# Optimization experiments

Measured on AMD Instinct MI355X. Metric: run time of the kernel, lower is better.

The kernel has to match this reference:

```python
import jax, jax.numpy as jnp
import numpy as np

EPS = 1e-6
NUM_HEADS = 8
NUM_TOKENS = 196

def setup_inputs() -> dict:
    key = jax.random.key(0)
    ks = jax.random.split(key, 4)
    B, N, C = 32, 3136, 384
    H, Dh, M = NUM_HEADS, C // NUM_HEADS, NUM_TOKENS
    return {
        "x": jax.random.normal(ks[0], (B, N, C), dtype=jnp.float32),
        "q_param": jax.random.normal(ks[1], (1, M, H, Dh), dtype=jnp.float32) * 0.02,
        "kv_w": jax.random.normal(ks[2], (2 * C, C), dtype=jnp.float32) * 0.02,
        "proj_w": jax.random.normal(ks[3], (C, C), dtype=jnp.float32) * 0.02,
        "proj_b": jnp.zeros((C,), dtype=jnp.float32),
        "ln_w": jnp.ones((C,), dtype=jnp.float32),
        "ln_b": jnp.zeros((C,), dtype=jnp.float32),
    }

def reference(x, q_param, kv_w, proj_w, proj_b, ln_w, ln_b):
    B, N, C = x.shape
    H = NUM_HEADS
    Dh = C // H
    # LayerNorm (eps=1e-6)
    mu = jnp.mean(x, axis=-1, keepdims=True)
    var = jnp.mean(jnp.square(x - mu), axis=-1, keepdims=True)
    x = (x - mu) * jax.lax.rsqrt(var + EPS) * ln_w + ln_b
    # exact GELU (nn.GELU default)
    x = jax.nn.gelu(x, approximate=False)
    # kv projection (no bias): [B,N,2C] -> k,v each [B,H,N,Dh]
    kv = (x @ kv_w.T).reshape(B, N, 2, H, Dh)
    kv = jnp.transpose(kv, (2, 0, 3, 1, 4))
    k, v = kv[0], kv[1]
    # learnable queries: (1,M,H,Dh) -> (1,H,M,Dh)
    q = jnp.transpose(q_param, (0, 2, 1, 3))
    # NOTE: source applies NO 1/sqrt(Dh) scaling
    attn = jnp.einsum("bhmd,bhnd->bhmn", jnp.broadcast_to(q, (B, H, NUM_TOKENS, Dh)), k)
    attn = jax.nn.softmax(attn, axis=-1)
    out = jnp.einsum("bhmn,bhnd->bhmd", attn, v)  # [B,H,M,Dh]
    out = jnp.transpose(out, (0, 2, 1, 3)).reshape(B, NUM_TOKENS, C)
    return out @ proj_w.T + proj_b
```

## Files before the change

### kernel.cpp

```cpp
#include <hip/hip_runtime.h>
#include <stdint.h>

typedef float f32x4 __attribute__((ext_vector_type(4)));
typedef short s16x8 __attribute__((ext_vector_type(8)));
typedef short s16x4 __attribute__((ext_vector_type(4)));
typedef unsigned short ushort_t;

#define B_  32
#define N_  3136
#define C_  384
#define H_  8
#define DH_ 48
#define M_  196
#define ROWS  (B_*N_)
#define PROWS (B_*M_)

static __device__ __forceinline__ ushort_t f2bf(float f) {
  union { float f; uint32_t u; } v; v.f = f;
  uint32_t r = (v.u + 0x7fffu + ((v.u >> 16) & 1u)) >> 16;
  return (ushort_t)r;
}
static __device__ __forceinline__ ushort_t f2bf_fast(float f) {
  union { float f; uint32_t u; } v; v.f = f;
  return (ushort_t)((v.u + 0x8000u) >> 16);
}

static __device__ __forceinline__ f32x4 mfma_16x16x32(s16x8 a, s16x8 b, f32x4 c) {
  return __builtin_amdgcn_mfma_f32_16x16x32_bf16(a, b, c, 0, 0, 0);
}

static __device__ __forceinline__ f32x4 mfma_16x16x16(s16x4 a, s16x4 b, f32x4 c) {
#if __has_builtin(__builtin_amdgcn_mfma_f32_16x16x16_bf16)
  return __builtin_amdgcn_mfma_f32_16x16x16_bf16(a, b, c, 0, 0, 0);
#elif __has_builtin(__builtin_amdgcn_mfma_f32_16x16x16bf16_1k)
  return __builtin_amdgcn_mfma_f32_16x16x16bf16_1k(a, b, c, 0, 0, 0);
#else
  f32x4 d;
  asm("v_mfma_f32_16x16x16_bf16 %0, %1, %2, %3" : "=v"(d) : "v"(a), "v"(b), "v"(c));
  return d;
#endif
}

static __device__ __forceinline__ void gload_lds16(const void* g, void* l) {
  __builtin_amdgcn_global_load_lds(
      (const __attribute__((address_space(1))) void*)(uintptr_t)g,
      (__attribute__((address_space(3))) void*)(uint32_t)(uintptr_t)l,
      16, 0, 0);
}

__global__ __launch_bounds__(256) void k_ln_gelu(
    const float* __restrict__ x, const float* __restrict__ lnw,
    const float* __restrict__ lnb, ushort_t* __restrict__ x16) {
  int row = blockIdx.x * 4 + (threadIdx.x >> 6);
  int lane = threadIdx.x & 63;
  const float2* xr = (const float2*)(x + (size_t)row * C_);
  float2 v0 = xr[lane], v1 = xr[lane + 64], v2 = xr[lane + 128];
  float s  = v0.x + v0.y + v1.x + v1.y + v2.x + v2.y;
  float ss = v0.x*v0.x + v0.y*v0.y + v1.x*v1.x + v1.y*v1.y + v2.x*v2.x + v2.y*v2.y;
#pragma unroll
  for (int off = 1; off < 64; off <<= 1) {
    s  += __shfl_xor(s, off);
    ss += __shfl_xor(ss, off);
  }
  float mu = s * (1.0f / C_);
  float rs = rsqrtf(ss * (1.0f / C_) - mu * mu + 1e-6f);
  const float2* wr = (const float2*)lnw;
  const float2* br = (const float2*)lnb;
  uint32_t* outp = (uint32_t*)(x16 + (size_t)row * C_);
#pragma unroll
  for (int t = 0; t < 3; ++t) {
    int idx = lane + t * 64;
    float2 v = (t == 0) ? v0 : ((t == 1) ? v1 : v2);
    float2 w = wr[idx], bb = br[idx];
    float a0 = (v.x - mu) * rs * w.x + bb.x;
    float a1 = (v.y - mu) * rs * w.y + bb.y;
    a0 = 0.5f * a0 * (1.0f + erff(a0 * 0.70710678118654752440f));
    a1 = 0.5f * a1 * (1.0f + erff(a1 * 0.70710678118654752440f));
    outp[idx] = (uint32_t)f2bf_fast(a0) | ((uint32_t)f2bf_fast(a1) << 16);
  }
}

__global__ __launch_bounds__(256) void k_convert(
    const float* __restrict__ kvw, const float* __restrict__ pw,
    const float* __restrict__ qp, ushort_t* __restrict__ wkv16,
    ushort_t* __restrict__ wp16, ushort_t* __restrict__ q16) {
  int i = blockIdx.x * 256 + threadIdx.x;
  if (i < 2 * C_ * C_) wkv16[i] = f2bf(kvw[i]);
  if (i < C_ * C_)     wp16[i]  = f2bf(pw[i]);
  if (i < M_ * H_ * DH_) {
    int d = i % DH_; int t = i / DH_; int h = t % H_; int m = t / H_;
    q16[((size_t)h * M_ + m) * DH_ + d] = f2bf(qp[i]);
  }
}

template <typename OutT, bool BIAS, bool SWZ>
__global__ __launch_bounds__(256) void k_gemm_bt(
    const ushort_t* __restrict__ A, const ushort_t* __restrict__ Bw,
    OutT* __restrict__ Co, const float* __restrict__ bias,
    int M, int N, int K, int ntn) {
  __shared__ ushort_t lA[3][128 * 32];
  __shared__ ushort_t lB[3][128 * 32];
  int bid = blockIdx.x;
  if (SWZ) bid = (bid & 7) * (gridDim.x >> 3) + (bid >> 3);
  int tr = bid / ntn, tc = bid % ntn;
  int tid = threadIdx.x;
  int w = tid >> 6, l = tid & 63;
  int wr = w >> 1, wc = w & 1;
  int c = l & 15, g = l >> 4;
  f32x4 acc[4][4];
#pragma unroll
  for (int i = 0; i < 4; ++i)
#pragma unroll
    for (int j = 0; j < 4; ++j) acc[i][j] = (f32x4){0.f, 0.f, 0.f, 0.f};
  const size_t a0 = (size_t)tr * 128, b0 = (size_t)tc * 128;
  int srow = l >> 2;
  int scol = (((l & 3) ^ ((l >> 3) & 3))) * 8;
  const int rsw = (c >> 1) & 3;
  const int T = K >> 5;
#pragma unroll
  for (int r = 0; r < 2; ++r) {
    int lr = w * 16 + r * 64;
    gload_lds16(A  + (a0 + lr + srow) * (size_t)K + scol, &lA[0][lr * 32]);
    gload_lds16(Bw + (b0 + lr + srow) * (size_t)K + scol, &lB[0][lr * 32]);
  }
  if (T > 1) {
#pragma unroll
    for (int r = 0; r < 2; ++r) {
      int lr = w * 16 + r * 64;
      gload_lds16(A  + (a0 + lr + srow) * (size_t)K + 32 + scol, &lA[1][lr * 32]);
      gload_lds16(Bw + (b0 + lr + srow) * (size_t)K + 32 + scol, &lB[1][lr * 32]);
    }
  }
  int cur = 0, nxt2 = 2;
  for (int t = 0; t < T; ++t) {
    if (t + 2 < T) {
      int kt = (t + 2) << 5;
#pragma unroll
      for (int r = 0; r < 2; ++r) {
        int lr = w * 16 + r * 64;
        gload_lds16(A  + (a0 + lr + srow) * (size_t)K + kt + scol, &lA[nxt2][lr * 32]);
        gload_lds16(Bw + (b0 + lr + srow) * (size_t)K + kt + scol, &lB[nxt2][lr * 32]);
      }
      asm volatile("s_waitcnt vmcnt(8)" ::: "memory");
    } else if (t + 1 < T) {
      asm volatile("s_waitcnt vmcnt(4)" ::: "memory");
    } else {
      asm volatile("s_waitcnt vmcnt(0)" ::: "memory");
    }
    __builtin_amdgcn_sched_barrier(0);
    __builtin_amdgcn_s_barrier();
    s16x8 af[4], bf[4];
#pragma unroll
    for (int i = 0; i < 4; ++i) {
      int row = wr * 64 + i * 16 + c;
      af[i] = *(const s16x8*)&lA[cur][row * 32 + ((unsigned)(g ^ rsw)) * 8];
    }
#pragma unroll
    for (int j = 0; j < 4; ++j) {
      int row = wc * 64 + j * 16 + c;
      bf[j] = *(const s16x8*)&lB[cur][row * 32 + ((unsigned)(g ^ rsw)) * 8];
    }
#pragma unroll
    for (int i = 0; i < 4; ++i)
#pragma unroll
      for (int j = 0; j < 4; ++j)
        acc[i][j] = mfma_16x16x32(af[i], bf[j], acc[i][j]);
    __builtin_amdgcn_sched_barrier(0);
    __builtin_amdgcn_s_barrier();
    cur = (cur == 2) ? 0 : cur + 1;
    nxt2 = (nxt2 == 2) ? 0 : nxt2 + 1;
  }
#pragma unroll
  for (int i = 0; i < 4; ++i) {
#pragma unroll
    for (int j = 0; j < 4; ++j) {
      size_t col = b0 + wc * 64 + j * 16 + c;
      float bs = BIAS ? bias[col] : 0.0f;
#pragma unroll
      for (int q = 0; q < 4; ++q) {
        size_t row = a0 + wr * 64 + i * 16 + g * 4 + q;
        float v = acc[i][j][q] + bs;
        if constexpr (sizeof(OutT) == 2) Co[row * N + col] = f2bf(v);
        else                             Co[row * N + col] = v;
      }
    }
  }
}

__global__ __launch_bounds__(256) void k_attn(
    const ushort_t* __restrict__ kv, const ushort_t* __restrict__ q16,
    ushort_t* __restrict__ att16) {
  int bh = blockIdx.x & 255, half = blockIdx.x >> 8;
  int b = bh >> 3, h = bh & 7;
  __shared__ ushort_t Kl[2][64 * 72];
  __shared__ ushort_t Vt[2][48 * 76];
  int tid = threadIdx.x;
  int w = tid >> 6, l = tid & 63;
  int c = l & 15, g = l >> 4;
  for (int i = tid; i < 2 * 64 * 72; i += 256) ((ushort_t*)Kl)[i] = 0;
  s16x8 qf[2][2];
#pragma unroll
  for (int i = 0; i < 2; ++i)
#pragma unroll
    for (int kk = 0; kk < 2; ++kk) {
      int m = half * 128 + w * 32 + i * 16 + c;
      int dh = kk * 32 + g * 8;
      s16x8 z = {0, 0, 0, 0, 0, 0, 0, 0};
      qf[i][kk] = (m < M_ && dh < DH_)
                      ? *(const s16x8*)(q16 + ((size_t)h * M_ + m) * DH_ + dh)
                      : z;
    }
  f32x4 o[3][2];
#pragma unroll
  for (int f = 0; f < 3; ++f)
#pragma unroll
    for (int i = 0; i < 2; ++i) o[f][i] = (f32x4){0.f, 0.f, 0.f, 0.f};
  float rm[2] = {-3e38f, -3e38f}, rl[2] = {0.f, 0.f};
  int srow = tid >> 2, spart = tid & 3;
  const size_t rowstride = (size_t)(2 * C_);
  const size_t gbase = (size_t)b * N_ * rowstride + h * DH_ + spart * 12;
  uint2 kA, kB, kC, vA, vB, vC;
  {
    const ushort_t* p = kv + gbase + (size_t)srow * rowstride;
    kA = *(const uint2*)(p);      kB = *(const uint2*)(p + 4);  kC = *(const uint2*)(p + 8);
    vA = *(const uint2*)(p + C_); vB = *(const uint2*)(p + C_ + 4); vC = *(const uint2*)(p + C_ + 8);
  }
  __syncthreads();

  for (int t = 0; t < 49; ++t) {
    int p = t & 1;
    uint2* kd = (uint2*)&Kl[p][srow * 72 + spart * 12];
    kd[0] = kA; kd[1] = kB; kd[2] = kC;
    int dbase = spart * 12;
    ushort_t* vt = &Vt[p][0];
    vt[(dbase + 0) * 76 + srow]  = (ushort_t)vA.x;
    vt[(dbase + 1) * 76 + srow]  = (ushort_t)(vA.x >> 16);
    vt[(dbase + 2) * 76 + srow]  = (ushort_t)vA.y;
    vt[(dbase + 3) * 76 + srow]  = (ushort_t)(vA.y >> 16);
    vt[(dbase + 4) * 76 + srow]  = (ushort_t)vB.x;
    vt[(dbase + 5) * 76 + srow]  = (ushort_t)(vB.x >> 16);
    vt[(dbase + 6) * 76 + srow]  = (ushort_t)vB.y;
    vt[(dbase + 7) * 76 + srow]  = (ushort_t)(vB.y >> 16);
    vt[(dbase + 8) * 76 + srow]  = (ushort_t)vC.x;
    vt[(dbase + 9) * 76 + srow]  = (ushort_t)(vC.x >> 16);
    vt[(dbase + 10) * 76 + srow] = (ushort_t)vC.y;
    vt[(dbase + 11) * 76 + srow] = (ushort_t)(vC.y >> 16);
    __syncthreads();
    {
      int tn = (t < 48) ? t + 1 : t;
      const ushort_t* pp = kv + gbase + ((size_t)tn * 64 + srow) * rowstride;
      kA = *(const uint2*)(pp);      kB = *(const uint2*)(pp + 4);  kC = *(const uint2*)(pp + 8);
      vA = *(const uint2*)(pp + C_); vB = *(const uint2*)(pp + C_ + 4); vC = *(const uint2*)(pp + C_ + 8);
    }
    f32x4 s[4][2];
    __builtin_amdgcn_s_setprio(1);
#pragma unroll
    for (int j = 0; j < 4; ++j) {
      s16x8 kf0 = *(const s16x8*)&Kl[p][(j * 16 + c) * 72 + g * 8];
      s16x8 kf1 = *(const s16x8*)&Kl[p][(j * 16 + c) * 72 + 32 + g * 8];
#pragma unroll
      for (int i = 0; i < 2; ++i) {
        f32x4 z = {0.f, 0.f, 0.f, 0.f};
        f32x4 t0 = mfma_16x16x32(kf0, qf[i][0], z);
        s[j][i] = mfma_16x16x32(kf1, qf[i][1], t0);
      }
    }
    __builtin_amdgcn_s_setprio(0);
    s16x4 pb[2][4];
#pragma unroll
    for (int i = 0; i < 2; ++i) {
      float tm = s[0][i][0];
#pragma unroll
      for (int j = 0; j < 4; ++j)
#pragma unroll
        for (int q = 0; q < 4; ++q) tm = fmaxf(tm, s[j][i][q]);
      tm = fmaxf(tm, __shfl_xor(tm, 16));
      tm = fmaxf(tm, __shfl_xor(tm, 32));
      float nm = fmaxf(rm[i], tm);
      float corr = __expf(rm[i] - nm);
      rm[i] = nm;
      float ts = 0.f;
#pragma unroll
      for (int j = 0; j < 4; ++j) {
        float p0 = __expf(s[j][i][0] - nm);
        float p1 = __expf(s[j][i][1] - nm);
        float p2 = __expf(s[j][i][2] - nm);
        float p3 = __expf(s[j][i][3] - nm);
        ts += (p0 + p1) + (p2 + p3);
        pb[i][j] = (s16x4){(short)f2bf_fast(p0), (short)f2bf_fast(p1),
                           (short)f2bf_fast(p2), (short)f2bf_fast(p3)};
      }
      ts += __shfl_xor(ts, 16);
      ts += __shfl_xor(ts, 32);
      rl[i] = rl[i] * corr + ts;
#pragma unroll
      for (int f = 0; f < 3; ++f) o[f][i] *= corr;
    }
    __builtin_amdgcn_s_setprio(1);
#pragma unroll
    for (int f = 0; f < 3; ++f)
#pragma unroll
      for (int j = 0; j < 4; ++j) {
        s16x4 vf = *(const s16x4*)&Vt[p][(f * 16 + c) * 76 + j * 16 + g * 4];
        o[f][0] = mfma_16x16x16(vf, pb[0][j], o[f][0]);
        o[f][1] = mfma_16x16x16(vf, pb[1][j], o[f][1]);
      }
    __builtin_amdgcn_s_setprio(0);
  }
#pragma unroll
  for (int i = 0; i < 2; ++i) {
    int m = half * 128 + w * 32 + i * 16 + c;
    if (m < M_) {
      float inv = 1.0f / rl[i];
#pragma unroll
      for (int f = 0; f < 3; ++f) {
        uint32_t w0 = (uint32_t)f2bf_fast(o[f][i][0] * inv) |
                      ((uint32_t)f2bf_fast(o[f][i][1] * inv) << 16);
        uint32_t w1 = (uint32_t)f2bf_fast(o[f][i][2] * inv) |
                      ((uint32_t)f2bf_fast(o[f][i][3] * inv) << 16);
        uint2 val; val.x = w0; val.y = w1;
        *(uint2*)&att16[((size_t)b * M_ + m) * C_ + h * DH_ + f * 16 + g * 4] = val;
      }
    }
  }
}

extern "C" void kernel_launch(void* const* d_in, const int* in_sizes, int n_in,
                              void* d_out, int out_size, void* d_ws, size_t ws_size,
                              hipStream_t stream) {
  (void)in_sizes; (void)n_in; (void)out_size; (void)ws_size;
  const float* x   = (const float*)d_in[0];
  const float* qp  = (const float*)d_in[1];
  const float* kvw = (const float*)d_in[2];
  const float* pw  = (const float*)d_in[3];
  const float* pbv = (const float*)d_in[4];
  const float* lnw = (const float*)d_in[5];
  const float* lnb = (const float*)d_in[6];
  float* out = (float*)d_out;

  ushort_t* x16   = (ushort_t*)d_ws;
  ushort_t* kv16  = x16 + (size_t)ROWS * C_;
  ushort_t* att16 = kv16 + (size_t)ROWS * 2 * C_;
  ushort_t* wkv16 = att16 + (size_t)PROWS * C_;
  ushort_t* wp16  = wkv16 + 2 * C_ * C_;
  ushort_t* q16   = wp16 + C_ * C_;

  hipLaunchKernelGGL(k_ln_gelu, dim3(ROWS / 4), dim3(256), 0, stream, x, lnw, lnb, x16);
  hipLaunchKernelGGL(k_convert, dim3((2 * C_ * C_ + 255) / 256), dim3(256), 0, stream,
                     kvw, pw, qp, wkv16, wp16, q16);
  hipLaunchKernelGGL((k_gemm_bt<ushort_t, false, true>),
                     dim3((ROWS / 128) * (2 * C_ / 128)), dim3(256), 0, stream,
                     x16, wkv16, kv16, (const float*)nullptr, ROWS, 2 * C_, C_, 2 * C_ / 128);
  hipLaunchKernelGGL(k_attn, dim3(B_ * H_ * 2), dim3(256), 0, stream, kv16, q16, att16);
  hipLaunchKernelGGL((k_gemm_bt<float, true, false>),
                     dim3((PROWS / 128) * (C_ / 128)), dim3(256), 0, stream,
                     att16, wp16, out, pbv, PROWS, C_, C_, C_ / 128);
}
```

Baseline: 259.9 us.

## Merge attention halves into 512-thread blocks with lazy softmax rescale

The attention kernel now launches one 512-thread block per (batch, head) in place of two 256-thread blocks, so all eight waves share a single K/V tile load into shared memory. Each thread moves a smaller slice of K/V. The online softmax skips the max update and the rescale of the accumulators unless the new max exceeds the running one by more than 8. Probabilities are packed to bf16 with the hardware v_cvt_pk_bf16_f32 instruction. The change halves redundant K/V global traffic but also halves the grid to 256 blocks, which may hurt occupancy.

```diff
diff --git a/kernel.cpp b/kernel.cpp
--- a/kernel.cpp
+++ b/kernel.cpp
@@ -23,6 +23,11 @@
 static __device__ __forceinline__ ushort_t f2bf_fast(float f) {
   union { float f; uint32_t u; } v; v.f = f;
   return (ushort_t)((v.u + 0x8000u) >> 16);
+}
+static __device__ __forceinline__ uint32_t pkbf(float lo, float hi) {
+  uint32_t r;
+  asm("v_cvt_pk_bf16_f32 %0, %1, %2" : "=v"(r) : "v"(lo), "v"(hi));
+  return r;
 }
 
 static __device__ __forceinline__ f32x4 mfma_16x16x32(s16x8 a, s16x8 b, f32x4 c) {
@@ -187,23 +192,23 @@
   }
 }
 
-__global__ __launch_bounds__(256) void k_attn(
+__global__ __launch_bounds__(512) void k_attn(
     const ushort_t* __restrict__ kv, const ushort_t* __restrict__ q16,
     ushort_t* __restrict__ att16) {
-  int bh = blockIdx.x & 255, half = blockIdx.x >> 8;
+  int bh = blockIdx.x;
   int b = bh >> 3, h = bh & 7;
   __shared__ ushort_t Kl[2][64 * 72];
   __shared__ ushort_t Vt[2][48 * 76];
   int tid = threadIdx.x;
   int w = tid >> 6, l = tid & 63;
   int c = l & 15, g = l >> 4;
-  for (int i = tid; i < 2 * 64 * 72; i += 256) ((ushort_t*)Kl)[i] = 0;
+  for (int i = tid; i < 2 * 64 * 72; i += 512) ((ushort_t*)Kl)[i] = 0;
   s16x8 qf[2][2];
 #pragma unroll
   for (int i = 0; i < 2; ++i)
 #pragma unroll
     for (int kk = 0; kk < 2; ++kk) {
-      int m = half * 128 + w * 32 + i * 16 + c;
+      int m = w * 32 + i * 16 + c;
       int dh = kk * 32 + g * 8;
       s16x8 z = {0, 0, 0, 0, 0, 0, 0, 0};
       qf[i][kk] = (m < M_ && dh < DH_)
@@ -216,41 +221,43 @@
 #pragma unroll
     for (int i = 0; i < 2; ++i) o[f][i] = (f32x4){0.f, 0.f, 0.f, 0.f};
   float rm[2] = {-3e38f, -3e38f}, rl[2] = {0.f, 0.f};
-  int srow = tid >> 2, spart = tid & 3;
+  int srow = tid >> 3, spart = tid & 7;
   const size_t rowstride = (size_t)(2 * C_);
-  const size_t gbase = (size_t)b * N_ * rowstride + h * DH_ + spart * 12;
-  uint2 kA, kB, kC, vA, vB, vC;
+  const size_t gbase = (size_t)b * N_ * rowstride + h * DH_ + spart * 6;
+  uint32_t kr0, kr1, kr2, vr0, vr1, vr2;
   {
     const ushort_t* p = kv + gbase + (size_t)srow * rowstride;
-    kA = *(const uint2*)(p);      kB = *(const uint2*)(p + 4);  kC = *(const uint2*)(p + 8);
-    vA = *(const uint2*)(p + C_); vB = *(const uint2*)(p + C_ + 4); vC = *(const uint2*)(p + C_ + 8);
+    kr0 = *(const uint32_t*)(p);
+    kr1 = *(const uint32_t*)(p + 2);
+    kr2 = *(const uint32_t*)(p + 4);
+    vr0 = *(const uint32_t*)(p + C_);
+    vr1 = *(const uint32_t*)(p + C_ + 2);
+    vr2 = *(const uint32_t*)(p + C_ + 4);
   }
   __syncthreads();
 
   for (int t = 0; t < 49; ++t) {
     int p = t & 1;
-    uint2* kd = (uint2*)&Kl[p][srow * 72 + spart * 12];
-    kd[0] = kA; kd[1] = kB; kd[2] = kC;
-    int dbase = spart * 12;
+    uint32_t* kd = (uint32_t*)&Kl[p][srow * 72 + spart * 6];
+    kd[0] = kr0; kd[1] = kr1; kd[2] = kr2;
+    int dbase = spart * 6;
     ushort_t* vt = &Vt[p][0];
-    vt[(dbase + 0) * 76 + srow]  = (ushort_t)vA.x;
-    vt[(dbase + 1) * 76 + srow]  = (ushort_t)(vA.x >> 16);
-    vt[(dbase + 2) * 76 + srow]  = (ushort_t)vA.y;
-    vt[(dbase + 3) * 76 + srow]  = (ushort_t)(vA.y >> 16);
-    vt[(dbase + 4) * 76 + srow]  = (ushort_t)vB.x;
-    vt[(dbase + 5) * 76 + srow]  = (ushort_t)(vB.x >> 16);
-    vt[(dbase + 6) * 76 + srow]  = (ushort_t)vB.y;
-    vt[(dbase + 7) * 76 + srow]  = (ushort_t)(vB.y >> 16);
-    vt[(dbase + 8) * 76 + srow]  = (ushort_t)vC.x;
-    vt[(dbase + 9) * 76 + srow]  = (ushort_t)(vC.x >> 16);
-    vt[(dbase + 10) * 76 + srow] = (ushort_t)vC.y;
-    vt[(dbase + 11) * 76 + srow] = (ushort_t)(vC.y >> 16);
+    vt[(dbase + 0) * 76 + srow] = (ushort_t)vr0;
+    vt[(dbase + 1) * 76 + srow] = (ushort_t)(vr0 >> 16);
+    vt[(dbase + 2) * 76 + srow] = (ushort_t)vr1;
+    vt[(dbase + 3) * 76 + srow] = (ushort_t)(vr1 >> 16);
+    vt[(dbase + 4) * 76 + srow] = (ushort_t)vr2;
+    vt[(dbase + 5) * 76 + srow] = (ushort_t)(vr2 >> 16);
     __syncthreads();
     {
       int tn = (t < 48) ? t + 1 : t;
       const ushort_t* pp = kv + gbase + ((size_t)tn * 64 + srow) * rowstride;
-      kA = *(const uint2*)(pp);      kB = *(const uint2*)(pp + 4);  kC = *(const uint2*)(pp + 8);
-      vA = *(const uint2*)(pp + C_); vB = *(const uint2*)(pp + C_ + 4); vC = *(const uint2*)(pp + C_ + 8);
+      kr0 = *(const uint32_t*)(pp);
+      kr1 = *(const uint32_t*)(pp + 2);
+      kr2 = *(const uint32_t*)(pp + 4);
+      vr0 = *(const uint32_t*)(pp + C_);
+      vr1 = *(const uint32_t*)(pp + C_ + 2);
+      vr2 = *(const uint32_t*)(pp + C_ + 4);
     }
     f32x4 s[4][2];
     __builtin_amdgcn_s_setprio(1);
@@ -276,25 +283,30 @@
         for (int q = 0; q < 4; ++q) tm = fmaxf(tm, s[j][i][q]);
       tm = fmaxf(tm, __shfl_xor(tm, 16));
       tm = fmaxf(tm, __shfl_xor(tm, 32));
-      float nm = fmaxf(rm[i], tm);
-      float corr = __expf(rm[i] - nm);
-      rm[i] = nm;
+      if (__any(tm > rm[i] + 8.f)) {
+        float nm = fmaxf(rm[i], tm);
+        float corr = __expf(rm[i] - nm);
+        rl[i] *= corr;
+#pragma unroll
+        for (int f = 0; f < 3; ++f) o[f][i] *= corr;
+        rm[i] = nm;
+      }
+      float m_i = rm[i];
       float ts = 0.f;
 #pragma unroll
       for (int j = 0; j < 4; ++j) {
-        float p0 = __expf(s[j][i][0] - nm);
-        float p1 = __expf(s[j][i][1] - nm);
-        float p2 = __expf(s[j][i][2] - nm);
-        float p3 = __expf(s[j][i][3] - nm);
+        float p0 = __expf(s[j][i][0] - m_i);
+        float p1 = __expf(s[j][i][1] - m_i);
+        float p2 = __expf(s[j][i][2] - m_i);
+        float p3 = __expf(s[j][i][3] - m_i);
         ts += (p0 + p1) + (p2 + p3);
-        pb[i][j] = (s16x4){(short)f2bf_fast(p0), (short)f2bf_fast(p1),
-                           (short)f2bf_fast(p2), (short)f2bf_fast(p3)};
+        uint32_t* pp = (uint32_t*)&pb[i][j];
+        pp[0] = pkbf(p0, p1);
+        pp[1] = pkbf(p2, p3);
       }
       ts += __shfl_xor(ts, 16);
       ts += __shfl_xor(ts, 32);
-      rl[i] = rl[i] * corr + ts;
-#pragma unroll
-      for (int f = 0; f < 3; ++f) o[f][i] *= corr;
+      rl[i] += ts;
     }
     __builtin_amdgcn_s_setprio(1);
 #pragma unroll
@@ -309,7 +321,7 @@
   }
 #pragma unroll
   for (int i = 0; i < 2; ++i) {
-    int m = half * 128 + w * 32 + i * 16 + c;
+    int m = w * 32 + i * 16 + c;
     if (m < M_) {
       float inv = 1.0f / rl[i];
 #pragma unroll
@@ -351,7 +363,7 @@
   hipLaunchKernelGGL((k_gemm_bt<ushort_t, false, true>),
                      dim3((ROWS / 128) * (2 * C_ / 128)), dim3(256), 0, stream,
                      x16, wkv16, kv16, (const float*)nullptr, ROWS, 2 * C_, C_, 2 * C_ / 128);
-  hipLaunchKernelGGL(k_attn, dim3(B_ * H_ * 2), dim3(256), 0, stream, kv16, q16, att16);
+  hipLaunchKernelGGL(k_attn, dim3(B_ * H_), dim3(512), 0, stream, kv16, q16, att16);
   hipLaunchKernelGGL((k_gemm_bt<float, true, false>),
                      dim3((PROWS / 128) * (C_ / 128)), dim3(256), 0, stream,
                      att16, wp16, out, pbv, PROWS, C_, C_, C_ / 128);
```

New measurement: 248.7 us. 1.05x faster.
